# Kernel optimization log

Measured on AMD Instinct MI355X. Metric: run time of the kernel, lower is better.

## Reference

```python
import jax, jax.numpy as jnp
import numpy as np

N = 400_000
B = 64          # number of segments (point clouds)
IN_C = 128
INTER = (256, 512, 512)
OUT_C = 512


def setup_inputs() -> dict:
    key = jax.random.key(0)
    ks = jax.random.split(key, 12)
    pos_emd = jax.random.normal(ks[0], (N, IN_C), dtype=jnp.float32)
    radius_p_batch = jnp.sort(jax.random.randint(ks[1], (N,), 0, B))

    def lin(k, fin, fout):
        kw, kb = jax.random.split(k)
        s = 1.0 / np.sqrt(fin)
        W = jax.random.uniform(kw, (fin, fout), jnp.float32, -s, s)
        b = jax.random.uniform(kb, (fout,), jnp.float32, -s, s)
        return W, b

    W1, b1 = lin(ks[2], IN_C, INTER[0])
    W2, b2 = lin(ks[3], INTER[0], INTER[1])
    W3, b3 = lin(ks[4], INTER[1], INTER[2])
    W4, b4 = lin(ks[5], IN_C + INTER[2], OUT_C)
    W5, b5 = lin(ks[6], OUT_C, OUT_C)
    return {
        "pos_emd": pos_emd, "radius_p_batch": radius_p_batch,
        "W1": W1, "b1": b1, "W2": W2, "b2": b2, "W3": W3, "b3": b3,
        "W4": W4, "b4": b4, "W5": W5, "b5": b5,
    }


def reference(pos_emd, radius_p_batch, W1, b1, W2, b2, W3, b3, W4, b4, W5, b5):
    # mlp1: Linear-ReLU-Linear-ReLU-Linear
    h = jax.nn.relu(pos_emd @ W1 + b1)
    h = jax.nn.relu(h @ W2 + b2)
    h = h @ W3 + b3                              # [N, 512]
    # global max pool over segments
    g = jax.ops.segment_max(h, radius_p_batch, num_segments=B)  # [B, 512]
    # broadcast each segment's global feature back to its points (ids sorted)
    g_rep = g[radius_p_batch]                    # [N, 512]
    z = jnp.concatenate((pos_emd, g_rep), axis=-1)  # [N, 640]
    # mlp2: Linear-ReLU-Linear
    z = jax.nn.relu(z @ W4 + b4)
    z = z @ W5 + b5                              # [N, 512]
    return jax.ops.segment_max(z, radius_p_batch, num_segments=B)  # [B, 512]
```

## Files before the change

kernel.cpp:

```cpp
#include <hip/hip_runtime.h>
#include <stdint.h>


typedef __bf16 bf16;
typedef __bf16 bf16x4 __attribute__((ext_vector_type(4)));
typedef __bf16 bf16x8 __attribute__((ext_vector_type(8)));
typedef float f32x4 __attribute__((ext_vector_type(4)));
typedef __attribute__((address_space(3))) char lds_char;

#define N_PTS 400000
#define ORD_NEG_INF 0x007FFFFFu

__device__ __forceinline__ unsigned f2ord(float f) {
  unsigned u = __float_as_uint(f);
  return (u & 0x80000000u) ? ~u : (u | 0x80000000u);
}
__device__ __forceinline__ float ord2f(unsigned o) {
  unsigned u = (o & 0x80000000u) ? (o ^ 0x80000000u) : ~o;
  return __uint_as_float(u);
}

__device__ __forceinline__ void gld16(const bf16* g, lds_char* l) {
  __builtin_amdgcn_global_load_lds((const __attribute__((address_space(1))) void*)g,
                                   (__attribute__((address_space(3))) void*)l, 16, 0, 0);
}

#define DSR(dst, preg, IMM) \
  asm volatile("ds_read_b128 %0, %1 offset:%c2" : "=&v"(dst) : "v"(preg), "n"(IMM))

#define SCHED0 __builtin_amdgcn_sched_barrier(0)
#define LGKM0 do { asm volatile("s_waitcnt lgkmcnt(0)"); SCHED0; } while (0)
#define LGKM2 do { asm volatile("s_waitcnt lgkmcnt(2)"); SCHED0; } while (0)
#define LGKM4 do { asm volatile("s_waitcnt lgkmcnt(4)"); SCHED0; } while (0)
#define LGKM6 do { asm volatile("s_waitcnt lgkmcnt(6)"); SCHED0; } while (0)
#define SBARR do { __builtin_amdgcn_s_barrier(); SCHED0; } while (0)
#define VMW4 do { asm volatile("s_waitcnt vmcnt(4)"); SCHED0; } while (0)
#define VMW0 do { asm volatile("s_waitcnt vmcnt(0)"); SCHED0; } while (0)

__global__ void k_init(unsigned* g_ord, unsigned* out_u) {
  int i = blockIdx.x * 256 + threadIdx.x;
  if (i < 64 * 512) { g_ord[i] = ORD_NEG_INF; out_u[i] = ORD_NEG_INF; }
}

__global__ void k_convX(const float* __restrict__ x, bf16* __restrict__ y, long n4) {
  long i = (long)blockIdx.x * 256 + threadIdx.x;
  long stride = (long)gridDim.x * 256;
  for (; i < n4; i += stride) {
    float4 v = ((const float4*)x)[i];
    bf16x4 o = {(bf16)v.x, (bf16)v.y, (bf16)v.z, (bf16)v.w};
    ((bf16x4*)y)[i] = o;
  }
}

__global__ void k_convWt(const float* __restrict__ W, bf16* __restrict__ Wt, int K, int Nout) {
  int idx = blockIdx.x * 256 + threadIdx.x;
  if (idx < K * Nout) {
    int k = idx / Nout, c = idx - k * Nout;
    Wt[(size_t)c * K + k] = (bf16)W[idx];
  }
}

__global__ void k_segbias(const unsigned* __restrict__ g_ord, const float* __restrict__ W4,
                          const float* __restrict__ b4, float* __restrict__ sb) {
  const int s = blockIdx.x, c = threadIdx.x;
  __shared__ float gs[512];
  gs[c] = ord2f(g_ord[s * 512 + c]);
  __syncthreads();
  float acc = b4[c];
  for (int j = 0; j < 512; ++j) acc = fmaf(gs[j], W4[(size_t)(128 + j) * 512 + c], acc);
  sb[s * 512 + c] = acc;
}

__global__ void k_decode(unsigned* p, int n) {
  int i = blockIdx.x * 256 + threadIdx.x;
  if (i < n) { float f = ord2f(p[i]); ((float*)p)[i] = f; }
}

template <int BIASMODE, bool RELU, int EPI, int K, int NOUT>
__launch_bounds__(512, 1)
__global__ void k_gemm(const bf16* __restrict__ A, const bf16* __restrict__ Bt,
                       const float* __restrict__ bias, const int* __restrict__ ids,
                       long row_off, bf16* __restrict__ out,
                       unsigned* __restrict__ outAtomic) {
  constexpr int NT = K / 64;
  constexpr int NIT = NT / 2;
  constexpr int NBX = NOUT / 256;
  __shared__ __align__(16) char sMem[131072];
  __shared__ int sIds[256];
  const int tid = threadIdx.x;
  const int wid = tid >> 6, lane = tid & 63;
  const int wr = wid >> 2, wc = wid & 3;
  const int lr = lane & 15, lk = lane >> 4;

  const int nwg = NBX * (int)gridDim.y;
  const int orig = (int)blockIdx.y * NBX + (int)blockIdx.x;
  const int q = nwg >> 3, r = nwg & 7;
  const int xcd = orig & 7, lid = orig >> 3;
  const int wg = (xcd < r ? xcd * (q + 1) : r * (q + 1) + (xcd - r) * q) + lid;
  const int n0 = (wg % NBX) * 256;
  const int m0 = (wg / NBX) * 256;

  if constexpr (BIASMODE == 1 || EPI == 1) {
    if (tid < 256) {
      long gi = row_off + m0 + tid;
      if (gi > (long)N_PTS - 1) gi = (long)N_PTS - 1;
      sIds[tid] = ids[gi];
    }
  }
  SCHED0;

  const int row0 = (wid * 2) * 8 + (lane >> 3);
  const int row1 = row0 + 8;
  const int sc0 = ((lane & 7) ^ (lane >> 4)) * 8;
  const int sc1 = ((lane & 7) ^ (4 + (lane >> 4))) * 8;
  lds_char* lds3 = (lds_char*)sMem;

  auto stageH = [&](int tau, int mat, int h) {
    if (tau >= NT) return;
    const int db = tau & 1;
    const bf16* srcb = (mat == 0) ? A + (size_t)(m0 + h * 128) * K
                                  : Bt + (size_t)(n0 + h * 128) * K;
    lds_char* d0 = lds3 + mat * 65536 + h * 32768 + db * 16384 + (wid * 2) * 1024;
    gld16(srcb + (size_t)row0 * K + tau * 64 + sc0, d0);
    gld16(srcb + (size_t)row1 * K + tau * 64 + sc1, d0 + 1024);
  };

  const unsigned s7 = (unsigned)(lr >> 1);
  const unsigned cks0 = (((unsigned)lk) ^ s7) * 16u;
  const unsigned cks1 = (((unsigned)lk + 4u) ^ s7) * 16u;
  lds_char* vA0 = lds3 + wr * 32768 + lr * 128 + cks0;
  lds_char* vA1 = lds3 + wr * 32768 + lr * 128 + cks1;
  lds_char* vB0 = lds3 + 65536 + (wc >> 1) * 32768 + (wc & 1) * 8192 + lr * 128 + cks0;
  lds_char* vB1 = lds3 + 65536 + (wc >> 1) * 32768 + (wc & 1) * 8192 + lr * 128 + cks1;

  bf16x8 aR[4][2], bR[4][2];
  f32x4 acc[8][4];
#pragma unroll
  for (int i = 0; i < 8; ++i)
#pragma unroll
    for (int j = 0; j < 4; ++j) acc[i][j] = {0.f, 0.f, 0.f, 0.f};

#define RD_A_K0(DB, IHI) do { \
  DSR(aR[0][0], vA0, (DB) + ((IHI) + 0) * 2048); DSR(aR[1][0], vA0, (DB) + ((IHI) + 1) * 2048); \
  DSR(aR[2][0], vA0, (DB) + ((IHI) + 2) * 2048); DSR(aR[3][0], vA0, (DB) + ((IHI) + 3) * 2048); \
} while (0)
#define RD_A_K1(DB, IHI) do { \
  DSR(aR[0][1], vA1, (DB) + ((IHI) + 0) * 2048); DSR(aR[1][1], vA1, (DB) + ((IHI) + 1) * 2048); \
  DSR(aR[2][1], vA1, (DB) + ((IHI) + 2) * 2048); DSR(aR[3][1], vA1, (DB) + ((IHI) + 3) * 2048); \
} while (0)
#define RD_B01_K0(DB) do { DSR(bR[0][0], vB0, (DB)); DSR(bR[1][0], vB0, (DB) + 2048); } while (0)
#define RD_B01_K1(DB) do { DSR(bR[0][1], vB1, (DB)); DSR(bR[1][1], vB1, (DB) + 2048); } while (0)
#define RD_B23_K0(DB) do { DSR(bR[2][0], vB0, (DB) + 4096); DSR(bR[3][0], vB0, (DB) + 6144); } while (0)
#define RD_B23_K1(DB) do { DSR(bR[2][1], vB1, (DB) + 4096); DSR(bR[3][1], vB1, (DB) + 6144); } while (0)
#define MMK(II, JJ, KK) do { __builtin_amdgcn_s_setprio(1); \
  _Pragma("unroll") for (int i_ = 0; i_ < 4; ++i_) \
  _Pragma("unroll") for (int j_ = 0; j_ < 2; ++j_) \
    acc[(II) + i_][(JJ) + j_] = __builtin_amdgcn_mfma_f32_16x16x32_bf16(aR[i_][KK], bR[(JJ) + j_][KK], acc[(II) + i_][(JJ) + j_], 0, 0, 0); \
  __builtin_amdgcn_s_setprio(0); } while (0)

  if constexpr (NIT == 1) {
    stageH(0, 1, 0); stageH(0, 1, 1); stageH(0, 0, 0); stageH(0, 0, 1);
    stageH(1, 1, 0); stageH(1, 1, 1); stageH(1, 0, 0); stageH(1, 0, 1);
    asm volatile("s_waitcnt vmcnt(0) lgkmcnt(0)");
    SCHED0;
    SBARR;
    RD_A_K0(0, 0); RD_B01_K0(0); RD_A_K1(0, 0); RD_B01_K1(0);
    LGKM6; MMK(0, 0, 0); LGKM0; MMK(0, 0, 1);
    RD_B23_K0(0); RD_B23_K1(0);
    LGKM2; MMK(0, 2, 0); LGKM0; MMK(0, 2, 1);
    RD_A_K0(0, 4); RD_A_K1(0, 4);
    LGKM4; MMK(4, 0, 0); LGKM0; MMK(4, 0, 1);
    MMK(4, 2, 0); MMK(4, 2, 1);
    RD_A_K0(16384, 0); RD_B01_K0(16384); RD_A_K1(16384, 0); RD_B01_K1(16384);
    LGKM6; MMK(0, 0, 0); LGKM0; MMK(0, 0, 1);
    RD_B23_K0(16384); RD_B23_K1(16384);
    LGKM2; MMK(0, 2, 0); LGKM0; MMK(0, 2, 1);
    RD_A_K0(16384, 4); RD_A_K1(16384, 4);
    LGKM4; MMK(4, 0, 0); LGKM0; MMK(4, 0, 1);
    MMK(4, 2, 0); MMK(4, 2, 1);
  } else {
    stageH(0, 1, 0); stageH(0, 1, 1); stageH(0, 0, 0); stageH(0, 0, 1);
    stageH(1, 1, 0); stageH(1, 1, 1);
    asm volatile("s_waitcnt vmcnt(4) lgkmcnt(0)");
    SCHED0;
    SBARR;

#pragma unroll 1
    for (int t = 0; t < NIT; ++t) {
      const int t2 = 2 * t;
      RD_A_K0(0, 0); RD_B01_K0(0);
      RD_A_K1(0, 0); RD_B01_K1(0);
      stageH(t2 + 1, 0, 0);
      LGKM6; MMK(0, 0, 0); LGKM0; MMK(0, 0, 1); SBARR;
      RD_B23_K0(0); RD_B23_K1(0);
      stageH(t2 + 1, 0, 1);
      LGKM2; MMK(0, 2, 0); LGKM0; MMK(0, 2, 1); SBARR;
      RD_A_K0(0, 4); RD_A_K1(0, 4);
      stageH(t2 + 2, 1, 0);
      LGKM4; MMK(4, 0, 0); LGKM0; MMK(4, 0, 1); SBARR;
      stageH(t2 + 2, 1, 1);
      MMK(4, 2, 0); MMK(4, 2, 1);
      if (t < NIT - 1) VMW4; else VMW0;
      SBARR;
      RD_A_K0(16384, 0); RD_B01_K0(16384);
      RD_A_K1(16384, 0); RD_B01_K1(16384);
      stageH(t2 + 2, 0, 0);
      LGKM6; MMK(0, 0, 0); LGKM0; MMK(0, 0, 1); SBARR;
      RD_B23_K0(16384); RD_B23_K1(16384);
      stageH(t2 + 2, 0, 1);
      LGKM2; MMK(0, 2, 0); LGKM0; MMK(0, 2, 1); SBARR;
      RD_A_K0(16384, 4); RD_A_K1(16384, 4);
      stageH(t2 + 3, 1, 0);
      LGKM4; MMK(4, 0, 0); LGKM0; MMK(4, 0, 1); SBARR;
      stageH(t2 + 3, 1, 1);
      MMK(4, 2, 0); MMK(4, 2, 1);
      if (t < NIT - 1) { VMW4; SBARR; }
    }
  }

  if constexpr (EPI == 0) {
#pragma unroll
    for (int j = 0; j < 4; ++j) {
      const int col = n0 + wc * 64 + j * 16 + lr;
      float bcol = (BIASMODE == 0) ? bias[col] : 0.f;
#pragma unroll
      for (int i = 0; i < 8; ++i) {
#pragma unroll
        for (int q2 = 0; q2 < 4; ++q2) {
          const int rl = wr * 128 + i * 16 + lk * 4 + q2;
          float v = acc[i][j][q2];
          if constexpr (BIASMODE == 0) v += bcol;
          else v += bias[(size_t)sIds[rl] * 512 + col];
          if constexpr (RELU) v = fmaxf(v, 0.f);
          out[(size_t)(m0 + rl) * NOUT + col] = (bf16)v;
        }
      }
    }
  } else {
    const int sLo = sIds[wr * 128], sHi = sIds[wr * 128 + 127];
#pragma unroll
    for (int j = 0; j < 4; ++j) {
      const int col = n0 + wc * 64 + j * 16 + lr;
      const float bcol = bias[col];
      for (int s = sLo; s <= sHi; ++s) {
        float m = -__builtin_inff();
#pragma unroll
        for (int i = 0; i < 8; ++i)
#pragma unroll
          for (int q2 = 0; q2 < 4; ++q2) {
            const int rl = wr * 128 + i * 16 + lk * 4 + q2;
            const bool rv = (row_off + m0 + rl) < (long)N_PTS;
            float v = acc[i][j][q2] + bcol;
            m = (sIds[rl] == s && rv) ? fmaxf(m, v) : m;
          }
        m = fmaxf(m, __shfl_xor(m, 16));
        m = fmaxf(m, __shfl_xor(m, 32));
        if (lane < 16) atomicMax(&outAtomic[(size_t)s * 512 + col], f2ord(m));
      }
    }
  }
#undef RD_A_K0
#undef RD_A_K1
#undef RD_B01_K0
#undef RD_B01_K1
#undef RD_B23_K0
#undef RD_B23_K1
#undef MMK
}

static inline long lmin(long a, long b) { return a < b ? a : b; }

extern "C" void kernel_launch(void* const* d_in, const int* in_sizes, int n_in,
                              void* d_out, int out_size, void* d_ws, size_t ws_size,
                              hipStream_t stream) {
  const float* pos = (const float*)d_in[0];
  const int* ids = (const int*)d_in[1];
  const float* W1 = (const float*)d_in[2]; const float* b1 = (const float*)d_in[3];
  const float* W2 = (const float*)d_in[4]; const float* b2 = (const float*)d_in[5];
  const float* W3 = (const float*)d_in[6]; const float* b3 = (const float*)d_in[7];
  const float* W4 = (const float*)d_in[8]; const float* b4 = (const float*)d_in[9];
  const float* W5 = (const float*)d_in[10]; const float* b5 = (const float*)d_in[11];

  char* ws = (char*)d_ws;
  size_t off = 0;
  auto alloc = [&](size_t bytes) -> char* {
    off = (off + 255) & ~(size_t)255;
    char* p = ws + off; off += bytes; return p;
  };
  bf16* Wt1  = (bf16*)alloc(128 * 256 * 2);
  bf16* Wt2  = (bf16*)alloc(256 * 512 * 2);
  bf16* Wt3  = (bf16*)alloc(512 * 512 * 2);
  bf16* Wt4a = (bf16*)alloc(128 * 512 * 2);
  bf16* Wt5  = (bf16*)alloc(512 * 512 * 2);
  unsigned* g_ord = (unsigned*)alloc(64 * 512 * 4);
  float* sb = (float*)alloc(64 * 512 * 4);
  bf16* Xbf = (bf16*)alloc((size_t)(N_PTS + 384) * 128 * 2);

  const size_t per_row = (256 + 512) * 2;
  size_t fixed_end = (off + 255) & ~(size_t)255;
  long avail = (long)ws_size - (long)fixed_end - 8192;
  long maxrows = avail / (long)per_row;
  long chunk = (maxrows - 256) & ~255L;
  if (chunk > N_PTS) chunk = N_PTS;
  if (chunk < 256) chunk = 256;
  long rows_alloc = chunk + 256;

  bf16* h1 = (bf16*)alloc((size_t)rows_alloc * 256 * 2);
  bf16* h2 = (bf16*)alloc((size_t)rows_alloc * 512 * 2);

  k_init<<<dim3(128), dim3(256), 0, stream>>>(g_ord, (unsigned*)d_out);
  k_convWt<<<dim3((128 * 256 + 255) / 256), dim3(256), 0, stream>>>(W1, Wt1, 128, 256);
  k_convWt<<<dim3((256 * 512 + 255) / 256), dim3(256), 0, stream>>>(W2, Wt2, 256, 512);
  k_convWt<<<dim3((512 * 512 + 255) / 256), dim3(256), 0, stream>>>(W3, Wt3, 512, 512);
  k_convWt<<<dim3((128 * 512 + 255) / 256), dim3(256), 0, stream>>>(W4, Wt4a, 128, 512);
  k_convWt<<<dim3((512 * 512 + 255) / 256), dim3(256), 0, stream>>>(W5, Wt5, 512, 512);
  k_convX<<<dim3(2048), dim3(256), 0, stream>>>(pos, Xbf, (long)N_PTS * 32);

  for (long o = 0; o < N_PTS; o += chunk) {
    long rows = lmin(chunk, N_PTS - o);
    unsigned mb = (unsigned)((rows + 255) / 256);
    k_gemm<0, true, 0, 128, 256><<<dim3(1, mb), dim3(512), 0, stream>>>(Xbf + o * 128, Wt1, b1, ids, o, h1, nullptr);
    k_gemm<0, true, 0, 256, 512><<<dim3(2, mb), dim3(512), 0, stream>>>(h1, Wt2, b2, ids, o, h2, nullptr);
    k_gemm<0, false, 1, 512, 512><<<dim3(2, mb), dim3(512), 0, stream>>>(h2, Wt3, b3, ids, o, nullptr, g_ord);
  }
  k_segbias<<<dim3(64), dim3(512), 0, stream>>>(g_ord, W4, b4, sb);
  for (long o = 0; o < N_PTS; o += chunk) {
    long rows = lmin(chunk, N_PTS - o);
    unsigned mb = (unsigned)((rows + 255) / 256);
    k_gemm<1, true, 0, 128, 512><<<dim3(2, mb), dim3(512), 0, stream>>>(Xbf + o * 128, Wt4a, sb, ids, o, h2, nullptr);
    k_gemm<0, false, 1, 512, 512><<<dim3(2, mb), dim3(512), 0, stream>>>(h2, Wt5, b5, ids, o, nullptr, (unsigned*)d_out);
  }
  k_decode<<<dim3(128), dim3(256), 0, stream>>>((unsigned*)d_out, 64 * 512);
}
```

Before: 1.093 ms.

## Make GEMM kernels persistent over M tiles with capped grid of 256 workgroups

Converts each GEMM launch into a persistent kernel. The grid is capped at 256 workgroups (matching the CU count) and each workgroup loops over M tiles with a stride of gridDim.y, with the XCD swizzle now applied only to the M index. The aim is to remove the tail effect when the number of tiles is not a multiple of the CU count, and to cut per-workgroup launch overhead. The trade-off is that the prologue can no longer overlap across tiles, which are processed serially within a workgroup, and a barrier is added between tiles.

```diff
diff --git a/kernel.cpp b/kernel.cpp
--- a/kernel.cpp
+++ b/kernel.cpp
@@ -81,10 +81,9 @@
 __global__ void k_gemm(const bf16* __restrict__ A, const bf16* __restrict__ Bt,
                        const float* __restrict__ bias, const int* __restrict__ ids,
                        long row_off, bf16* __restrict__ out,
-                       unsigned* __restrict__ outAtomic) {
+                       unsigned* __restrict__ outAtomic, int MT) {
   constexpr int NT = K / 64;
   constexpr int NIT = NT / 2;
-  constexpr int NBX = NOUT / 256;
   __shared__ __align__(16) char sMem[131072];
   __shared__ int sIds[256];
   const int tid = threadIdx.x;
@@ -92,28 +91,19 @@
   const int wr = wid >> 2, wc = wid & 3;
   const int lr = lane & 15, lk = lane >> 4;
 
-  const int nwg = NBX * (int)gridDim.y;
-  const int orig = (int)blockIdx.y * NBX + (int)blockIdx.x;
-  const int q = nwg >> 3, r = nwg & 7;
-  const int xcd = orig & 7, lid = orig >> 3;
-  const int wg = (xcd < r ? xcd * (q + 1) : r * (q + 1) + (xcd - r) * q) + lid;
-  const int n0 = (wg % NBX) * 256;
-  const int m0 = (wg / NBX) * 256;
-
-  if constexpr (BIASMODE == 1 || EPI == 1) {
-    if (tid < 256) {
-      long gi = row_off + m0 + tid;
-      if (gi > (long)N_PTS - 1) gi = (long)N_PTS - 1;
-      sIds[tid] = ids[gi];
-    }
-  }
-  SCHED0;
+  const int n0 = (int)blockIdx.x * 256;
+  const int GY = (int)gridDim.y;
+  const int q = GY >> 3, r = GY & 7;
+  const int y = (int)blockIdx.y;
+  const int xcd = y & 7, lid = y >> 3;
+  const int swzY = (xcd < r ? xcd * (q + 1) : r * (q + 1) + (xcd - r) * q) + lid;
 
   const int row0 = (wid * 2) * 8 + (lane >> 3);
   const int row1 = row0 + 8;
   const int sc0 = ((lane & 7) ^ (lane >> 4)) * 8;
   const int sc1 = ((lane & 7) ^ (4 + (lane >> 4))) * 8;
   lds_char* lds3 = (lds_char*)sMem;
+  int m0 = 0;
 
   auto stageH = [&](int tau, int mat, int h) {
     if (tau >= NT) return;
@@ -135,10 +125,6 @@
 
   bf16x8 aR[4][2], bR[4][2];
   f32x4 acc[8][4];
-#pragma unroll
-  for (int i = 0; i < 8; ++i)
-#pragma unroll
-    for (int j = 0; j < 4; ++j) acc[i][j] = {0.f, 0.f, 0.f, 0.f};
 
 #define RD_A_K0(DB, IHI) do { \
   DSR(aR[0][0], vA0, (DB) + ((IHI) + 0) * 2048); DSR(aR[1][0], vA0, (DB) + ((IHI) + 1) * 2048); \
@@ -158,106 +144,123 @@
     acc[(II) + i_][(JJ) + j_] = __builtin_amdgcn_mfma_f32_16x16x32_bf16(aR[i_][KK], bR[(JJ) + j_][KK], acc[(II) + i_][(JJ) + j_], 0, 0, 0); \
   __builtin_amdgcn_s_setprio(0); } while (0)
 
-  if constexpr (NIT == 1) {
-    stageH(0, 1, 0); stageH(0, 1, 1); stageH(0, 0, 0); stageH(0, 0, 1);
-    stageH(1, 1, 0); stageH(1, 1, 1); stageH(1, 0, 0); stageH(1, 0, 1);
-    asm volatile("s_waitcnt vmcnt(0) lgkmcnt(0)");
+#pragma unroll 1
+  for (int mt = swzY; mt < MT; mt += GY) {
+    m0 = mt * 256;
+    if constexpr (BIASMODE == 1 || EPI == 1) {
+      if (tid < 256) {
+        long gi = row_off + m0 + tid;
+        if (gi > (long)N_PTS - 1) gi = (long)N_PTS - 1;
+        sIds[tid] = ids[gi];
+      }
+    }
     SCHED0;
-    SBARR;
-    RD_A_K0(0, 0); RD_B01_K0(0); RD_A_K1(0, 0); RD_B01_K1(0);
-    LGKM6; MMK(0, 0, 0); LGKM0; MMK(0, 0, 1);
-    RD_B23_K0(0); RD_B23_K1(0);
-    LGKM2; MMK(0, 2, 0); LGKM0; MMK(0, 2, 1);
-    RD_A_K0(0, 4); RD_A_K1(0, 4);
-    LGKM4; MMK(4, 0, 0); LGKM0; MMK(4, 0, 1);
-    MMK(4, 2, 0); MMK(4, 2, 1);
-    RD_A_K0(16384, 0); RD_B01_K0(16384); RD_A_K1(16384, 0); RD_B01_K1(16384);
-    LGKM6; MMK(0, 0, 0); LGKM0; MMK(0, 0, 1);
-    RD_B23_K0(16384); RD_B23_K1(16384);
-    LGKM2; MMK(0, 2, 0); LGKM0; MMK(0, 2, 1);
-    RD_A_K0(16384, 4); RD_A_K1(16384, 4);
-    LGKM4; MMK(4, 0, 0); LGKM0; MMK(4, 0, 1);
-    MMK(4, 2, 0); MMK(4, 2, 1);
-  } else {
-    stageH(0, 1, 0); stageH(0, 1, 1); stageH(0, 0, 0); stageH(0, 0, 1);
-    stageH(1, 1, 0); stageH(1, 1, 1);
-    asm volatile("s_waitcnt vmcnt(4) lgkmcnt(0)");
-    SCHED0;
-    SBARR;
-
+#pragma unroll
+    for (int i = 0; i < 8; ++i)
+#pragma unroll
+      for (int j = 0; j < 4; ++j) acc[i][j] = {0.f, 0.f, 0.f, 0.f};
+
+    if constexpr (NIT == 1) {
+      stageH(0, 1, 0); stageH(0, 1, 1); stageH(0, 0, 0); stageH(0, 0, 1);
+      stageH(1, 1, 0); stageH(1, 1, 1); stageH(1, 0, 0); stageH(1, 0, 1);
+      asm volatile("s_waitcnt vmcnt(0) lgkmcnt(0)");
+      SCHED0;
+      SBARR;
+      RD_A_K0(0, 0); RD_B01_K0(0); RD_A_K1(0, 0); RD_B01_K1(0);
+      LGKM6; MMK(0, 0, 0); LGKM0; MMK(0, 0, 1);
+      RD_B23_K0(0); RD_B23_K1(0);
+      LGKM2; MMK(0, 2, 0); LGKM0; MMK(0, 2, 1);
+      RD_A_K0(0, 4); RD_A_K1(0, 4);
+      LGKM4; MMK(4, 0, 0); LGKM0; MMK(4, 0, 1);
+      MMK(4, 2, 0); MMK(4, 2, 1);
+      RD_A_K0(16384, 0); RD_B01_K0(16384); RD_A_K1(16384, 0); RD_B01_K1(16384);
+      LGKM6; MMK(0, 0, 0); LGKM0; MMK(0, 0, 1);
+      RD_B23_K0(16384); RD_B23_K1(16384);
+      LGKM2; MMK(0, 2, 0); LGKM0; MMK(0, 2, 1);
+      RD_A_K0(16384, 4); RD_A_K1(16384, 4);
+      LGKM4; MMK(4, 0, 0); LGKM0; MMK(4, 0, 1);
+      MMK(4, 2, 0); MMK(4, 2, 1);
+    } else {
+      stageH(0, 1, 0); stageH(0, 1, 1); stageH(0, 0, 0); stageH(0, 0, 1);
+      stageH(1, 1, 0); stageH(1, 1, 1);
+      asm volatile("s_waitcnt vmcnt(4) lgkmcnt(0)");
+      SCHED0;
+      SBARR;
 #pragma unroll 1
-    for (int t = 0; t < NIT; ++t) {
-      const int t2 = 2 * t;
-      RD_A_K0(0, 0); RD_B01_K0(0);
-      RD_A_K1(0, 0); RD_B01_K1(0);
-      stageH(t2 + 1, 0, 0);
-      LGKM6; MMK(0, 0, 0); LGKM0; MMK(0, 0, 1); SBARR;
-      RD_B23_K0(0); RD_B23_K1(0);
-      stageH(t2 + 1, 0, 1);
-      LGKM2; MMK(0, 2, 0); LGKM0; MMK(0, 2, 1); SBARR;
-      RD_A_K0(0, 4); RD_A_K1(0, 4);
-      stageH(t2 + 2, 1, 0);
-      LGKM4; MMK(4, 0, 0); LGKM0; MMK(4, 0, 1); SBARR;
-      stageH(t2 + 2, 1, 1);
-      MMK(4, 2, 0); MMK(4, 2, 1);
-      if (t < NIT - 1) VMW4; else VMW0;
-      SBARR;
-      RD_A_K0(16384, 0); RD_B01_K0(16384);
-      RD_A_K1(16384, 0); RD_B01_K1(16384);
-      stageH(t2 + 2, 0, 0);
-      LGKM6; MMK(0, 0, 0); LGKM0; MMK(0, 0, 1); SBARR;
-      RD_B23_K0(16384); RD_B23_K1(16384);
-      stageH(t2 + 2, 0, 1);
-      LGKM2; MMK(0, 2, 0); LGKM0; MMK(0, 2, 1); SBARR;
-      RD_A_K0(16384, 4); RD_A_K1(16384, 4);
-      stageH(t2 + 3, 1, 0);
-      LGKM4; MMK(4, 0, 0); LGKM0; MMK(4, 0, 1); SBARR;
-      stageH(t2 + 3, 1, 1);
-      MMK(4, 2, 0); MMK(4, 2, 1);
-      if (t < NIT - 1) { VMW4; SBARR; }
+      for (int t = 0; t < NIT; ++t) {
+        const int t2 = 2 * t;
+        RD_A_K0(0, 0); RD_B01_K0(0);
+        RD_A_K1(0, 0); RD_B01_K1(0);
+        stageH(t2 + 1, 0, 0);
+        LGKM6; MMK(0, 0, 0); LGKM0; MMK(0, 0, 1); SBARR;
+        RD_B23_K0(0); RD_B23_K1(0);
+        stageH(t2 + 1, 0, 1);
+        LGKM2; MMK(0, 2, 0); LGKM0; MMK(0, 2, 1); SBARR;
+        RD_A_K0(0, 4); RD_A_K1(0, 4);
+        stageH(t2 + 2, 1, 0);
+        LGKM4; MMK(4, 0, 0); LGKM0; MMK(4, 0, 1); SBARR;
+        stageH(t2 + 2, 1, 1);
+        MMK(4, 2, 0); MMK(4, 2, 1);
+        if (t < NIT - 1) VMW4; else VMW0;
+        SBARR;
+        RD_A_K0(16384, 0); RD_B01_K0(16384);
+        RD_A_K1(16384, 0); RD_B01_K1(16384);
+        stageH(t2 + 2, 0, 0);
+        LGKM6; MMK(0, 0, 0); LGKM0; MMK(0, 0, 1); SBARR;
+        RD_B23_K0(16384); RD_B23_K1(16384);
+        stageH(t2 + 2, 0, 1);
+        LGKM2; MMK(0, 2, 0); LGKM0; MMK(0, 2, 1); SBARR;
+        RD_A_K0(16384, 4); RD_A_K1(16384, 4);
+        stageH(t2 + 3, 1, 0);
+        LGKM4; MMK(4, 0, 0); LGKM0; MMK(4, 0, 1); SBARR;
+        stageH(t2 + 3, 1, 1);
+        MMK(4, 2, 0); MMK(4, 2, 1);
+        if (t < NIT - 1) { VMW4; SBARR; }
+      }
     }
-  }
-
-  if constexpr (EPI == 0) {
-#pragma unroll
-    for (int j = 0; j < 4; ++j) {
-      const int col = n0 + wc * 64 + j * 16 + lr;
-      float bcol = (BIASMODE == 0) ? bias[col] : 0.f;
-#pragma unroll
-      for (int i = 0; i < 8; ++i) {
-#pragma unroll
-        for (int q2 = 0; q2 < 4; ++q2) {
-          const int rl = wr * 128 + i * 16 + lk * 4 + q2;
-          float v = acc[i][j][q2];
-          if constexpr (BIASMODE == 0) v += bcol;
-          else v += bias[(size_t)sIds[rl] * 512 + col];
-          if constexpr (RELU) v = fmaxf(v, 0.f);
-          out[(size_t)(m0 + rl) * NOUT + col] = (bf16)v;
+
+    if constexpr (EPI == 0) {
+#pragma unroll
+      for (int j = 0; j < 4; ++j) {
+        const int col = n0 + wc * 64 + j * 16 + lr;
+        float bcol = (BIASMODE == 0) ? bias[col] : 0.f;
+#pragma unroll
+        for (int i = 0; i < 8; ++i) {
+#pragma unroll
+          for (int q2 = 0; q2 < 4; ++q2) {
+            const int rl = wr * 128 + i * 16 + lk * 4 + q2;
+            float v = acc[i][j][q2];
+            if constexpr (BIASMODE == 0) v += bcol;
+            else v += bias[(size_t)sIds[rl] * 512 + col];
+            if constexpr (RELU) v = fmaxf(v, 0.f);
+            out[(size_t)(m0 + rl) * NOUT + col] = (bf16)v;
+          }
+        }
+      }
+    } else {
+      const int sLo = sIds[wr * 128], sHi = sIds[wr * 128 + 127];
+#pragma unroll
+      for (int j = 0; j < 4; ++j) {
+        const int col = n0 + wc * 64 + j * 16 + lr;
+        const float bcol = bias[col];
+        for (int s = sLo; s <= sHi; ++s) {
+          float m = -__builtin_inff();
+#pragma unroll
+          for (int i = 0; i < 8; ++i)
+#pragma unroll
+            for (int q2 = 0; q2 < 4; ++q2) {
+              const int rl = wr * 128 + i * 16 + lk * 4 + q2;
+              const bool rv = (row_off + m0 + rl) < (long)N_PTS;
+              float v = acc[i][j][q2] + bcol;
+              m = (sIds[rl] == s && rv) ? fmaxf(m, v) : m;
+            }
+          m = fmaxf(m, __shfl_xor(m, 16));
+          m = fmaxf(m, __shfl_xor(m, 32));
+          if (lane < 16) atomicMax(&outAtomic[(size_t)s * 512 + col], f2ord(m));
         }
       }
     }
-  } else {
-    const int sLo = sIds[wr * 128], sHi = sIds[wr * 128 + 127];
-#pragma unroll
-    for (int j = 0; j < 4; ++j) {
-      const int col = n0 + wc * 64 + j * 16 + lr;
-      const float bcol = bias[col];
-      for (int s = sLo; s <= sHi; ++s) {
-        float m = -__builtin_inff();
-#pragma unroll
-        for (int i = 0; i < 8; ++i)
-#pragma unroll
-          for (int q2 = 0; q2 < 4; ++q2) {
-            const int rl = wr * 128 + i * 16 + lk * 4 + q2;
-            const bool rv = (row_off + m0 + rl) < (long)N_PTS;
-            float v = acc[i][j][q2] + bcol;
-            m = (sIds[rl] == s && rv) ? fmaxf(m, v) : m;
-          }
-        m = fmaxf(m, __shfl_xor(m, 16));
-        m = fmaxf(m, __shfl_xor(m, 32));
-        if (lane < 16) atomicMax(&outAtomic[(size_t)s * 512 + col], f2ord(m));
-      }
-    }
+    if (mt + GY < MT) SBARR;
   }
 #undef RD_A_K0
 #undef RD_A_K1
@@ -316,19 +319,29 @@
   k_convWt<<<dim3((512 * 512 + 255) / 256), dim3(256), 0, stream>>>(W5, Wt5, 512, 512);
   k_convX<<<dim3(2048), dim3(256), 0, stream>>>(pos, Xbf, (long)N_PTS * 32);
 
+  auto gy = [](int mb, int nbx) -> unsigned {
+    int cap = 256 / nbx;
+    return (unsigned)(mb < cap ? mb : cap);
+  };
+
   for (long o = 0; o < N_PTS; o += chunk) {
     long rows = lmin(chunk, N_PTS - o);
-    unsigned mb = (unsigned)((rows + 255) / 256);
-    k_gemm<0, true, 0, 128, 256><<<dim3(1, mb), dim3(512), 0, stream>>>(Xbf + o * 128, Wt1, b1, ids, o, h1, nullptr);
-    k_gemm<0, true, 0, 256, 512><<<dim3(2, mb), dim3(512), 0, stream>>>(h1, Wt2, b2, ids, o, h2, nullptr);
-    k_gemm<0, false, 1, 512, 512><<<dim3(2, mb), dim3(512), 0, stream>>>(h2, Wt3, b3, ids, o, nullptr, g_ord);
+    int mb = (int)((rows + 255) / 256);
+    k_gemm<0, true, 0, 128, 256><<<dim3(1, gy(mb, 1)), dim3(512), 0, stream>>>(
+        Xbf + o * 128, Wt1, b1, ids, o, h1, nullptr, mb);
+    k_gemm<0, true, 0, 256, 512><<<dim3(2, gy(mb, 2)), dim3(512), 0, stream>>>(
+        h1, Wt2, b2, ids, o, h2, nullptr, mb);
+    k_gemm<0, false, 1, 512, 512><<<dim3(2, gy(mb, 2)), dim3(512), 0, stream>>>(
+        h2, Wt3, b3, ids, o, nullptr, g_ord, mb);
   }
   k_segbias<<<dim3(64), dim3(512), 0, stream>>>(g_ord, W4, b4, sb);
   for (long o = 0; o < N_PTS; o += chunk) {
     long rows = lmin(chunk, N_PTS - o);
-    unsigned mb = (unsigned)((rows + 255) / 256);
-    k_gemm<1, true, 0, 128, 512><<<dim3(2, mb), dim3(512), 0, stream>>>(Xbf + o * 128, Wt4a, sb, ids, o, h2, nullptr);
-    k_gemm<0, false, 1, 512, 512><<<dim3(2, mb), dim3(512), 0, stream>>>(h2, Wt5, b5, ids, o, nullptr, (unsigned*)d_out);
+    int mb = (int)((rows + 255) / 256);
+    k_gemm<1, true, 0, 128, 512><<<dim3(2, gy(mb, 2)), dim3(512), 0, stream>>>(
+        Xbf + o * 128, Wt4a, sb, ids, o, h2, nullptr, mb);
+    k_gemm<0, false, 1, 512, 512><<<dim3(2, gy(mb, 2)), dim3(512), 0, stream>>>(
+        h2, Wt5, b5, ids, o, nullptr, (unsigned*)d_out, mb);
   }
   k_decode<<<dim3(128), dim3(256), 0, stream>>>((unsigned*)d_out, 64 * 512);
 }
```

Measured after the change: 1.390 ms. +27.2%, slower.
